# Performance work log

Measured on AMD Instinct MI355X. Metric: run time of the kernel, lower is better.

Reference implementation:

```python
import jax, jax.numpy as jnp
import numpy as np

N = 50000   # in_size (nodes)
E = 400000  # edges per network
H = 4       # n_heads
D = 64      # dimension per head
M = 3       # n_modalities


def setup_inputs() -> dict:
    key = jax.random.key(0)
    ks = jax.random.split(key, 10)
    return {
        "x": jax.random.normal(ks[0], (N, H * D), dtype=jnp.float32),
        "edge_index_0": jax.random.randint(ks[1], (2, E), 0, N, dtype=jnp.int32),
        "edge_index_1": jax.random.randint(ks[2], (2, E), 0, N, dtype=jnp.int32),
        "edge_index_2": jax.random.randint(ks[3], (2, E), 0, N, dtype=jnp.int32),
        "attn_0": jax.random.uniform(ks[4], (E, H), dtype=jnp.float32),
        "attn_1": jax.random.uniform(ks[5], (E, H), dtype=jnp.float32),
        "attn_2": jax.random.uniform(ks[6], (E, H), dtype=jnp.float32),
        "net_weights": jax.random.uniform(ks[7], (M,), dtype=jnp.float32),
        "lin_weight": jax.random.normal(ks[8], (H * D, H * D), dtype=jnp.float32) * (1.0 / np.sqrt(H * D)),
        "bias": jnp.zeros((H * D,), dtype=jnp.float32),
    }


def reference(x, edge_index_0, edge_index_1, edge_index_2,
              attn_0, attn_1, attn_2, net_weights, lin_weight, bias):
    # --- aggregat_edge_weights: per-network scalar weight * per-edge attention,
    # combined into one sparse COO attention matrix. Coalescing (summing duplicate
    # edges) is deferred to the scatter-add below, which is mathematically identical.
    edges = jnp.concatenate([edge_index_0, edge_index_1, edge_index_2], axis=1)  # [2, 3E]
    alpha = jnp.concatenate([
        net_weights[0] * attn_0,
        net_weights[1] * attn_1,
        net_weights[2] * attn_2,
    ], axis=0)  # [3E, H]

    # --- CoAttnWGATConv with precomputed alpha (no self-loops):
    # project, reshape to heads, gather source messages, scale by alpha, scatter-sum.
    xp = (x @ lin_weight).reshape(N, H, D)          # [N, H, D]
    src, dst = edges[0], edges[1]
    msgs = xp[src] * alpha[:, :, None]              # [3E, H, D]
    out = jax.ops.segment_sum(msgs, dst, num_segments=N)  # [N, H, D]
    return out.reshape(N, H * D) + bias
```

## Files before the change

### kernel.cpp

```cpp
#include <hip/hip_runtime.h>

#define N_NODES 50000
#define N_EDGES 400000
#define TOT_E   (3 * N_EDGES)
#define CH      256
#define NHEADS  4
#define BUCKET  64

#define FILL_BLOCKS ((TOT_E + 255) / 256)
#define GEMM_BLOCKS (((N_NODES + 63) / 64) * 4)

typedef __attribute__((ext_vector_type(8))) short short8v;
typedef __attribute__((ext_vector_type(8))) unsigned short ushort8v;
typedef __attribute__((ext_vector_type(4))) float float4v;

__device__ inline unsigned short f2b(float f) {
  union { float f; unsigned u; } x; x.f = f;
  return (unsigned short)((x.u + 0x7FFFu + ((x.u >> 16) & 1u)) >> 16);
}
__device__ inline float b2f(unsigned short s) {
  union { unsigned u; float f; } x; x.u = ((unsigned)s) << 16;
  return x.f;
}
__device__ inline float h2f(unsigned short s) {
  return (float)__builtin_bit_cast(_Float16, s);
}
__device__ inline unsigned short f2h(float f) {
  return __builtin_bit_cast(unsigned short, (_Float16)f);
}

__global__ __launch_bounds__(256) void prep_kernel(
    const float* __restrict__ W, unsigned short* __restrict__ WTp) {
  int i = blockIdx.x * 256 + threadIdx.x;
  int f = i >> 9, ks = (i >> 6) & 7, l = i & 63;
  int lr = l & 15, lk = l >> 4;
  unsigned short* dst = WTp + (size_t)i * 8;
  #pragma unroll
  for (int j = 0; j < 8; ++j)
    dst[j] = f2b(W[(ks * 32 + lk * 8 + j) * 256 + f * 16 + lr]);
}

__global__ __launch_bounds__(256) void fused_kernel(
    const int* __restrict__ e0, const int* __restrict__ e1,
    const int* __restrict__ e2,
    const float* __restrict__ a0, const float* __restrict__ a1,
    const float* __restrict__ a2, const float* __restrict__ nw,
    int* __restrict__ cursor, int4* __restrict__ recs,
    const float* __restrict__ x, const unsigned short* __restrict__ WTp,
    unsigned short* __restrict__ xpb) {
  if (blockIdx.x < FILL_BLOCKS) {
    int g = blockIdx.x * 256 + threadIdx.x;
    if (g >= TOT_E) return;
    int net = (g >= 2 * N_EDGES) ? 2 : (g >= N_EDGES ? 1 : 0);
    int e = g - net * N_EDGES;
    const int* ei = (net == 0) ? e0 : (net == 1 ? e1 : e2);
    const float* at = (net == 0) ? a0 : (net == 1 ? a1 : a2);
    const float wv = nw[net];
    int src = ei[e];
    int dst = ei[N_EDGES + e];
    float4 al = *(const float4*)(at + (size_t)e * NHEADS);
    int4 rec;
    rec.x = src;
    rec.y = ((int)f2h(wv * al.y) << 16) | (int)f2h(wv * al.x);
    rec.z = ((int)f2h(wv * al.w) << 16) | (int)f2h(wv * al.z);
    rec.w = 0;
    int pos = atomicAdd(&cursor[dst], 1);
    if (pos < BUCKET) recs[(size_t)dst * BUCKET + pos] = rec;
  } else {
    const int gb = blockIdx.x - FILL_BLOCKS;
    const int fbase = (gb & 3) * 4;
    const int xtile = gb >> 2;
    const int tid = threadIdx.x;
    const int w = tid >> 6;
    const int l = tid & 63;
    const int lr = l & 15, lk = l >> 4;
    const int xrow = xtile * 64 + w * 16 + lr;
    const bool valid = (xrow < N_NODES);
    const short8v* __restrict__ wp = (const short8v*)WTp;

    float4v acc[4];
    #pragma unroll
    for (int f = 0; f < 4; ++f) acc[f] = (float4v)0.0f;

    for (int ks = 0; ks < 8; ++ks) {
      short8v b;
      if (valid) {
        const float4* px = (const float4*)(x + (size_t)xrow * 256 + ks * 32 + lk * 8);
        float4 u0 = px[0], u1 = px[1];
        b[0]=(short)f2b(u0.x); b[1]=(short)f2b(u0.y); b[2]=(short)f2b(u0.z); b[3]=(short)f2b(u0.w);
        b[4]=(short)f2b(u1.x); b[5]=(short)f2b(u1.y); b[6]=(short)f2b(u1.z); b[7]=(short)f2b(u1.w);
      } else {
        b = (short8v)0;
      }
      #pragma unroll
      for (int f = 0; f < 4; ++f) {
        short8v a = wp[((fbase + f) * 8 + ks) * 64 + l];
        acc[f] = __builtin_amdgcn_mfma_f32_16x16x32_bf16(a, b, acc[f], 0, 0, 0);
      }
    }

    if (valid) {
      unsigned short* rowp = xpb + (size_t)xrow * 256 + lk * 4;
      #pragma unroll
      for (int f = 0; f < 4; ++f) {
        ushort4 pk;
        pk.x = f2b(acc[f][0]);
        pk.y = f2b(acc[f][1]);
        pk.z = f2b(acc[f][2]);
        pk.w = f2b(acc[f][3]);
        *(ushort4*)(rowp + (fbase + f) * 16) = pk;
      }
    }
  }
}

__global__ __launch_bounds__(256) void gather_kernel(
    const int4* __restrict__ recs, const int* __restrict__ cursor,
    const unsigned short* __restrict__ xpb, const float* __restrict__ bias,
    float* __restrict__ out) {
  const int wid = (blockIdx.x * 256 + threadIdx.x) >> 6;
  const int lane = threadIdx.x & 63;
  const int half = lane >> 5;
  const int l = lane & 31;
  const int n = wid * 2 + half;
  const int c = l * 8;
  const int h = l >> 3;

  const int cnt = min(cursor[n], BUCKET);
  const int4* __restrict__ rp = recs + (size_t)n * BUCKET;

  float acc[8] = {};
  int i = 0;
  for (; i + 4 <= cnt; i += 4) {
    int4 r0 = rp[i + 0], r1 = rp[i + 1], r2 = rp[i + 2], r3 = rp[i + 3];
    unsigned w0 = (h & 2) ? (unsigned)r0.z : (unsigned)r0.y;
    unsigned w1 = (h & 2) ? (unsigned)r1.z : (unsigned)r1.y;
    unsigned w2 = (h & 2) ? (unsigned)r2.z : (unsigned)r2.y;
    unsigned w3 = (h & 2) ? (unsigned)r3.z : (unsigned)r3.y;
    float A0 = h2f((unsigned short)((h & 1) ? (w0 >> 16) : (w0 & 0xffff)));
    float A1 = h2f((unsigned short)((h & 1) ? (w1 >> 16) : (w1 & 0xffff)));
    float A2 = h2f((unsigned short)((h & 1) ? (w2 >> 16) : (w2 & 0xffff)));
    float A3 = h2f((unsigned short)((h & 1) ? (w3 >> 16) : (w3 & 0xffff)));
    ushort8v v0 = *(const ushort8v*)(xpb + (size_t)r0.x * CH + c);
    ushort8v v1 = *(const ushort8v*)(xpb + (size_t)r1.x * CH + c);
    ushort8v v2 = *(const ushort8v*)(xpb + (size_t)r2.x * CH + c);
    ushort8v v3 = *(const ushort8v*)(xpb + (size_t)r3.x * CH + c);
    #pragma unroll
    for (int j = 0; j < 8; ++j) {
      acc[j] += A0 * b2f(v0[j]) + A1 * b2f(v1[j]) +
                A2 * b2f(v2[j]) + A3 * b2f(v3[j]);
    }
  }
  for (; i < cnt; ++i) {
    int4 r = rp[i];
    unsigned wd = (h & 2) ? (unsigned)r.z : (unsigned)r.y;
    float A = h2f((unsigned short)((h & 1) ? (wd >> 16) : (wd & 0xffff)));
    ushort8v v = *(const ushort8v*)(xpb + (size_t)r.x * CH + c);
    #pragma unroll
    for (int j = 0; j < 8; ++j) acc[j] += A * b2f(v[j]);
  }

  const float4 b0 = *(const float4*)(bias + c);
  const float4 b1 = *(const float4*)(bias + c + 4);
  float* o = out + (size_t)n * CH + c;
  *(float4*)(o + 0) = make_float4(acc[0] + b0.x, acc[1] + b0.y, acc[2] + b0.z, acc[3] + b0.w);
  *(float4*)(o + 4) = make_float4(acc[4] + b1.x, acc[5] + b1.y, acc[6] + b1.z, acc[7] + b1.w);
}

extern "C" void kernel_launch(void* const* d_in, const int* in_sizes, int n_in,
                              void* d_out, int out_size, void* d_ws, size_t ws_size,
                              hipStream_t stream) {
  const float* x    = (const float*)d_in[0];
  const int*   e0   = (const int*)d_in[1];
  const int*   e1   = (const int*)d_in[2];
  const int*   e2   = (const int*)d_in[3];
  const float* a0   = (const float*)d_in[4];
  const float* a1   = (const float*)d_in[5];
  const float* a2   = (const float*)d_in[6];
  const float* nw   = (const float*)d_in[7];
  const float* W    = (const float*)d_in[8];
  const float* bias = (const float*)d_in[9];
  float* out = (float*)d_out;

  char* ws = (char*)d_ws;
  size_t o = 0;
  unsigned short* xpb = (unsigned short*)(ws + o); o += (size_t)N_NODES * CH * 2;
  int4* recs = (int4*)(ws + o);                    o += (size_t)N_NODES * BUCKET * 16;
  unsigned short* WTp = (unsigned short*)(ws + o); o += 65536 * 2;
  int* cursor = (int*)(ws + o);                    o += (size_t)N_NODES * 4;

  hipMemsetAsync(cursor, 0, (size_t)N_NODES * 4, stream);
  prep_kernel<<<32, 256, 0, stream>>>(W, WTp);
  fused_kernel<<<FILL_BLOCKS + GEMM_BLOCKS, 256, 0, stream>>>(
      e0, e1, e2, a0, a1, a2, nw, cursor, recs, x, WTp, xpb);
  gather_kernel<<<N_NODES / 8, 256, 0, stream>>>(recs, cursor, xpb, bias, out);
}
```

Baseline: 215.4 us.

## Split fused fill/GEMM kernel, widen GEMM tile, fold memset, predicate gather tail

```diff
diff --git a/kernel.cpp b/kernel.cpp
--- a/kernel.cpp
+++ b/kernel.cpp
@@ -6,9 +6,6 @@
 #define CH      256
 #define NHEADS  4
 #define BUCKET  64
-
-#define FILL_BLOCKS ((TOT_E + 255) / 256)
-#define GEMM_BLOCKS (((N_NODES + 63) / 64) * 4)
 
 typedef __attribute__((ext_vector_type(8))) short short8v;
 typedef __attribute__((ext_vector_type(8))) unsigned short ushort8v;
@@ -30,88 +27,90 @@
 }
 
 __global__ __launch_bounds__(256) void prep_kernel(
-    const float* __restrict__ W, unsigned short* __restrict__ WTp) {
+    const float* __restrict__ W, unsigned short* __restrict__ WTp,
+    int* __restrict__ cursor) {
   int i = blockIdx.x * 256 + threadIdx.x;
-  int f = i >> 9, ks = (i >> 6) & 7, l = i & 63;
-  int lr = l & 15, lk = l >> 4;
-  unsigned short* dst = WTp + (size_t)i * 8;
-  #pragma unroll
-  for (int j = 0; j < 8; ++j)
-    dst[j] = f2b(W[(ks * 32 + lk * 8 + j) * 256 + f * 16 + lr]);
+  if (i < N_NODES) cursor[i] = 0;
+  if (i < 8192) {
+    int f = i >> 9, ks = (i >> 6) & 7, l = i & 63;
+    int lr = l & 15, lk = l >> 4;
+    unsigned short* dst = WTp + (size_t)i * 8;
+    #pragma unroll
+    for (int j = 0; j < 8; ++j)
+      dst[j] = f2b(W[(ks * 32 + lk * 8 + j) * 256 + f * 16 + lr]);
+  }
 }
 
-__global__ __launch_bounds__(256) void fused_kernel(
+__global__ __launch_bounds__(256) void gemm_kernel(
+    const float* __restrict__ x, const unsigned short* __restrict__ WTp,
+    unsigned short* __restrict__ xpb) {
+  const int tid = threadIdx.x;
+  const int w = tid >> 6;
+  const int l = tid & 63;
+  const int lr = l & 15, lk = l >> 4;
+  const int xrow = blockIdx.x * 64 + w * 16 + lr;
+  const int fbase = blockIdx.y * 8;
+  const bool valid = (xrow < N_NODES);
+  const short8v* __restrict__ wp = (const short8v*)WTp;
+
+  float4v acc[8];
+  #pragma unroll
+  for (int f = 0; f < 8; ++f) acc[f] = (float4v)0.0f;
+
+  for (int ks = 0; ks < 8; ++ks) {
+    short8v b;
+    if (valid) {
+      const float4* px = (const float4*)(x + (size_t)xrow * 256 + ks * 32 + lk * 8);
+      float4 u0 = px[0], u1 = px[1];
+      b[0]=(short)f2b(u0.x); b[1]=(short)f2b(u0.y); b[2]=(short)f2b(u0.z); b[3]=(short)f2b(u0.w);
+      b[4]=(short)f2b(u1.x); b[5]=(short)f2b(u1.y); b[6]=(short)f2b(u1.z); b[7]=(short)f2b(u1.w);
+    } else {
+      b = (short8v)0;
+    }
+    #pragma unroll
+    for (int f = 0; f < 8; ++f) {
+      short8v a = wp[((fbase + f) * 8 + ks) * 64 + l];
+      acc[f] = __builtin_amdgcn_mfma_f32_16x16x32_bf16(a, b, acc[f], 0, 0, 0);
+    }
+  }
+
+  if (valid) {
+    unsigned short* rowp = xpb + (size_t)xrow * 256 + lk * 4;
+    #pragma unroll
+    for (int f = 0; f < 8; ++f) {
+      ushort4 pk;
+      pk.x = f2b(acc[f][0]);
+      pk.y = f2b(acc[f][1]);
+      pk.z = f2b(acc[f][2]);
+      pk.w = f2b(acc[f][3]);
+      *(ushort4*)(rowp + (fbase + f) * 16) = pk;
+    }
+  }
+}
+
+__global__ __launch_bounds__(256) void fill_kernel(
     const int* __restrict__ e0, const int* __restrict__ e1,
     const int* __restrict__ e2,
     const float* __restrict__ a0, const float* __restrict__ a1,
     const float* __restrict__ a2, const float* __restrict__ nw,
-    int* __restrict__ cursor, int4* __restrict__ recs,
-    const float* __restrict__ x, const unsigned short* __restrict__ WTp,
-    unsigned short* __restrict__ xpb) {
-  if (blockIdx.x < FILL_BLOCKS) {
-    int g = blockIdx.x * 256 + threadIdx.x;
-    if (g >= TOT_E) return;
-    int net = (g >= 2 * N_EDGES) ? 2 : (g >= N_EDGES ? 1 : 0);
-    int e = g - net * N_EDGES;
-    const int* ei = (net == 0) ? e0 : (net == 1 ? e1 : e2);
-    const float* at = (net == 0) ? a0 : (net == 1 ? a1 : a2);
-    const float wv = nw[net];
-    int src = ei[e];
-    int dst = ei[N_EDGES + e];
-    float4 al = *(const float4*)(at + (size_t)e * NHEADS);
-    int4 rec;
-    rec.x = src;
-    rec.y = ((int)f2h(wv * al.y) << 16) | (int)f2h(wv * al.x);
-    rec.z = ((int)f2h(wv * al.w) << 16) | (int)f2h(wv * al.z);
-    rec.w = 0;
-    int pos = atomicAdd(&cursor[dst], 1);
-    if (pos < BUCKET) recs[(size_t)dst * BUCKET + pos] = rec;
-  } else {
-    const int gb = blockIdx.x - FILL_BLOCKS;
-    const int fbase = (gb & 3) * 4;
-    const int xtile = gb >> 2;
-    const int tid = threadIdx.x;
-    const int w = tid >> 6;
-    const int l = tid & 63;
-    const int lr = l & 15, lk = l >> 4;
-    const int xrow = xtile * 64 + w * 16 + lr;
-    const bool valid = (xrow < N_NODES);
-    const short8v* __restrict__ wp = (const short8v*)WTp;
-
-    float4v acc[4];
-    #pragma unroll
-    for (int f = 0; f < 4; ++f) acc[f] = (float4v)0.0f;
-
-    for (int ks = 0; ks < 8; ++ks) {
-      short8v b;
-      if (valid) {
-        const float4* px = (const float4*)(x + (size_t)xrow * 256 + ks * 32 + lk * 8);
-        float4 u0 = px[0], u1 = px[1];
-        b[0]=(short)f2b(u0.x); b[1]=(short)f2b(u0.y); b[2]=(short)f2b(u0.z); b[3]=(short)f2b(u0.w);
-        b[4]=(short)f2b(u1.x); b[5]=(short)f2b(u1.y); b[6]=(short)f2b(u1.z); b[7]=(short)f2b(u1.w);
-      } else {
-        b = (short8v)0;
-      }
-      #pragma unroll
-      for (int f = 0; f < 4; ++f) {
-        short8v a = wp[((fbase + f) * 8 + ks) * 64 + l];
-        acc[f] = __builtin_amdgcn_mfma_f32_16x16x32_bf16(a, b, acc[f], 0, 0, 0);
-      }
-    }
-
-    if (valid) {
-      unsigned short* rowp = xpb + (size_t)xrow * 256 + lk * 4;
-      #pragma unroll
-      for (int f = 0; f < 4; ++f) {
-        ushort4 pk;
-        pk.x = f2b(acc[f][0]);
-        pk.y = f2b(acc[f][1]);
-        pk.z = f2b(acc[f][2]);
-        pk.w = f2b(acc[f][3]);
-        *(ushort4*)(rowp + (fbase + f) * 16) = pk;
-      }
-    }
-  }
+    int* __restrict__ cursor, int4* __restrict__ recs) {
+  int g = blockIdx.x * 256 + threadIdx.x;
+  if (g >= TOT_E) return;
+  int net = (g >= 2 * N_EDGES) ? 2 : (g >= N_EDGES ? 1 : 0);
+  int e = g - net * N_EDGES;
+  const int* ei = (net == 0) ? e0 : (net == 1 ? e1 : e2);
+  const float* at = (net == 0) ? a0 : (net == 1 ? a1 : a2);
+  const float wv = nw[net];
+  int src = ei[e];
+  int dst = ei[N_EDGES + e];
+  float4 al = *(const float4*)(at + (size_t)e * NHEADS);
+  int4 rec;
+  rec.x = src;
+  rec.y = ((int)f2h(wv * al.y) << 16) | (int)f2h(wv * al.x);
+  rec.z = ((int)f2h(wv * al.w) << 16) | (int)f2h(wv * al.z);
+  rec.w = 0;
+  int pos = atomicAdd(&cursor[dst], 1);
+  if (pos < BUCKET) recs[(size_t)dst * BUCKET + pos] = rec;
 }
 
 __global__ __launch_bounds__(256) void gather_kernel(
@@ -130,34 +129,30 @@
   const int4* __restrict__ rp = recs + (size_t)n * BUCKET;
 
   float acc[8] = {};
-  int i = 0;
-  for (; i + 4 <= cnt; i += 4) {
+  for (int i = 0; i < cnt; i += 4) {
     int4 r0 = rp[i + 0], r1 = rp[i + 1], r2 = rp[i + 2], r3 = rp[i + 3];
+    const bool p1 = (i + 1) < cnt, p2 = (i + 2) < cnt, p3 = (i + 3) < cnt;
+    const int s0 = r0.x;
+    const int s1 = p1 ? r1.x : 0;
+    const int s2 = p2 ? r2.x : 0;
+    const int s3 = p3 ? r3.x : 0;
     unsigned w0 = (h & 2) ? (unsigned)r0.z : (unsigned)r0.y;
     unsigned w1 = (h & 2) ? (unsigned)r1.z : (unsigned)r1.y;
     unsigned w2 = (h & 2) ? (unsigned)r2.z : (unsigned)r2.y;
     unsigned w3 = (h & 2) ? (unsigned)r3.z : (unsigned)r3.y;
     float A0 = h2f((unsigned short)((h & 1) ? (w0 >> 16) : (w0 & 0xffff)));
-    float A1 = h2f((unsigned short)((h & 1) ? (w1 >> 16) : (w1 & 0xffff)));
-    float A2 = h2f((unsigned short)((h & 1) ? (w2 >> 16) : (w2 & 0xffff)));
-    float A3 = h2f((unsigned short)((h & 1) ? (w3 >> 16) : (w3 & 0xffff)));
-    ushort8v v0 = *(const ushort8v*)(xpb + (size_t)r0.x * CH + c);
-    ushort8v v1 = *(const ushort8v*)(xpb + (size_t)r1.x * CH + c);
-    ushort8v v2 = *(const ushort8v*)(xpb + (size_t)r2.x * CH + c);
-    ushort8v v3 = *(const ushort8v*)(xpb + (size_t)r3.x * CH + c);
+    float A1 = p1 ? h2f((unsigned short)((h & 1) ? (w1 >> 16) : (w1 & 0xffff))) : 0.0f;
+    float A2 = p2 ? h2f((unsigned short)((h & 1) ? (w2 >> 16) : (w2 & 0xffff))) : 0.0f;
+    float A3 = p3 ? h2f((unsigned short)((h & 1) ? (w3 >> 16) : (w3 & 0xffff))) : 0.0f;
+    ushort8v v0 = *(const ushort8v*)(xpb + (size_t)s0 * CH + c);
+    ushort8v v1 = *(const ushort8v*)(xpb + (size_t)s1 * CH + c);
+    ushort8v v2 = *(const ushort8v*)(xpb + (size_t)s2 * CH + c);
+    ushort8v v3 = *(const ushort8v*)(xpb + (size_t)s3 * CH + c);
     #pragma unroll
     for (int j = 0; j < 8; ++j) {
       acc[j] += A0 * b2f(v0[j]) + A1 * b2f(v1[j]) +
                 A2 * b2f(v2[j]) + A3 * b2f(v3[j]);
     }
-  }
-  for (; i < cnt; ++i) {
-    int4 r = rp[i];
-    unsigned wd = (h & 2) ? (unsigned)r.z : (unsigned)r.y;
-    float A = h2f((unsigned short)((h & 1) ? (wd >> 16) : (wd & 0xffff)));
-    ushort8v v = *(const ushort8v*)(xpb + (size_t)r.x * CH + c);
-    #pragma unroll
-    for (int j = 0; j < 8; ++j) acc[j] += A * b2f(v[j]);
   }
 
   const float4 b0 = *(const float4*)(bias + c);
@@ -189,9 +184,12 @@
   unsigned short* WTp = (unsigned short*)(ws + o); o += 65536 * 2;
   int* cursor = (int*)(ws + o);                    o += (size_t)N_NODES * 4;
 
-  hipMemsetAsync(cursor, 0, (size_t)N_NODES * 4, stream);
-  prep_kernel<<<32, 256, 0, stream>>>(W, WTp);
-  fused_kernel<<<FILL_BLOCKS + GEMM_BLOCKS, 256, 0, stream>>>(
-      e0, e1, e2, a0, a1, a2, nw, cursor, recs, x, WTp, xpb);
+  const int nNodeBlk = (N_NODES + 255) / 256;
+  const int nEdgeBlk = (TOT_E + 255) / 256;
+
+  prep_kernel<<<nNodeBlk, 256, 0, stream>>>(W, WTp, cursor);
+  gemm_kernel<<<dim3((N_NODES + 63) / 64, 2), 256, 0, stream>>>(x, WTp, xpb);
+  fill_kernel<<<nEdgeBlk, 256, 0, stream>>>(e0, e1, e2, a0, a1, a2, nw,
+                                            cursor, recs);
   gather_kernel<<<N_NODES / 8, 256, 0, stream>>>(recs, cursor, xpb, bias, out);
 }
```

After: 199.4 us (median of 3 runs). 1.08x faster.
